# Kernel optimization log

Measured on AMD Instinct MI355X. Metric: run time of the kernel, lower is better.

The kernel has to match this reference:

```python
import jax, jax.numpy as jnp
import numpy as np

D_MODEL = 512
NHEAD = 8
HEAD_DIM = D_MODEL // NHEAD


def setup_inputs() -> dict:
    key = jax.random.key(0)
    k1, k2, k3, k4, k5 = jax.random.split(key, 5)
    x = jax.random.normal(k1, (4, 2048, D_MODEL), dtype=jnp.float32)
    s = 1.0 / np.sqrt(D_MODEL)
    W_qkv = jax.random.normal(k2, (D_MODEL, 3 * D_MODEL), dtype=jnp.float32) * s
    b_qkv = jax.random.normal(k3, (3 * D_MODEL,), dtype=jnp.float32) * 0.01
    W_fc = jax.random.normal(k4, (D_MODEL, D_MODEL), dtype=jnp.float32) * s
    b_fc = jax.random.normal(k5, (D_MODEL,), dtype=jnp.float32) * 0.01
    return {"x": x, "W_qkv": W_qkv, "b_qkv": b_qkv, "W_fc": W_fc, "b_fc": b_fc}


def reference(x, W_qkv, b_qkv, W_fc, b_fc):
    b, t, _ = x.shape
    qkv = x @ W_qkv + b_qkv                      # [b, t, 3*d]
    q, k, v = jnp.split(qkv, 3, axis=-1)
    def heads(a):
        return a.reshape(b, t, NHEAD, HEAD_DIM).transpose(0, 2, 1, 3)  # b h t d
    q, k, v = heads(q), heads(k), heads(v)
    scale = HEAD_DIM ** -0.5
    dots = jnp.einsum('bhid,bhjd->bhij', q, k) * scale
    attn = jax.nn.softmax(dots, axis=-1)         # dropout = identity (eval)
    out = jnp.einsum('bhij,bhjd->bhid', attn, v)
    out = out.transpose(0, 2, 1, 3).reshape(b, t, D_MODEL)
    return out @ W_fc + b_fc
```

## Files before the change

kernel.cpp:

```cpp
#include <hip/hip_runtime.h>
#include <hip/hip_bf16.h>
#include <cstddef>
#include <cstdint>

typedef __bf16 bf16_t;
typedef __attribute__((ext_vector_type(8))) __bf16 bf16x8;
typedef __attribute__((ext_vector_type(4))) float f32x4;
typedef __attribute__((ext_vector_type(16))) float f32x16;
typedef __attribute__((ext_vector_type(2))) unsigned uint2v;

#define B_   4
#define T_   2048
#define D_   512
#define H_   8
#define HD_  64
#define BT_  8192
#define N3_  1536

__device__ inline f32x4 mfma16(bf16x8 a, bf16x8 b, f32x4 c) {
  return __builtin_amdgcn_mfma_f32_16x16x32_bf16(a, b, c, 0, 0, 0);
}
__device__ inline f32x16 mfma32(bf16x8 a, bf16x8 b, f32x16 c) {
  return __builtin_amdgcn_mfma_f32_32x32x16_bf16(a, b, c, 0, 0, 0);
}

#define GLOADLDS(lds_base, gsrc)                                           \
  __builtin_amdgcn_global_load_lds(                                        \
      (const __attribute__((address_space(1))) unsigned int*)(gsrc),       \
      (__attribute__((address_space(3))) unsigned int*)(lds_base), 16, 0, 0)


__global__ __launch_bounds__(256) void k_castx(const float* __restrict__ in,
                                               bf16_t* __restrict__ out) {
  const size_t i = ((size_t)blockIdx.x * 256 + threadIdx.x) * 8;
  f32x4 v0 = *reinterpret_cast<const f32x4*>(&in[i]);
  f32x4 v1 = *reinterpret_cast<const f32x4*>(&in[i + 4]);
  bf16x8 o;
#pragma unroll
  for (int k = 0; k < 4; ++k) { o[k] = (bf16_t)v0[k]; o[4 + k] = (bf16_t)v1[k]; }
  *reinterpret_cast<bf16x8*>(&out[i]) = o;
}

__global__ __launch_bounds__(256) void k_tcast(const float* __restrict__ in,
                                               bf16_t* __restrict__ out,
                                               int R, int C) {
  __shared__ bf16_t tile[64][72];
  const int c0 = blockIdx.x * 64, r0 = blockIdx.y * 64;
  const int t = threadIdx.x;
  const int rr = t >> 4;
  const int cc = (t & 15) * 4;
#pragma unroll
  for (int p = 0; p < 4; ++p) {
    int r = p * 16 + rr;
    f32x4 v = *reinterpret_cast<const f32x4*>(&in[(size_t)(r0 + r) * C + c0 + cc]);
#pragma unroll
    for (int i = 0; i < 4; ++i) tile[cc + i][r] = (bf16_t)v[i];
  }
  __syncthreads();
#pragma unroll
  for (int p = 0; p < 4; ++p) {
    int c = p * 16 + rr;
    union { uint2 u; bf16_t e[4]; } pk;
#pragma unroll
    for (int i = 0; i < 4; ++i) pk.e[i] = tile[c][cc + i];
    *reinterpret_cast<uint2*>(&out[(size_t)(c0 + c) * R + r0 + cc]) = pk.u;
  }
}

__global__ __launch_bounds__(512) void k_gemm_qkv(
    const bf16_t* __restrict__ Xb, const bf16_t* __restrict__ Wt,
    const float* __restrict__ bias, bf16_t* __restrict__ Qp,
    bf16_t* __restrict__ Kp, bf16_t* __restrict__ Vp) {
  __shared__ __align__(16) char smem[34816];
  bf16_t* As = (bf16_t*)smem;
  bf16_t* Bs = (bf16_t*)(smem + 16384);
  const int bm0 = blockIdx.x * 128, bn0 = blockIdx.y * 128;
  const int tid = threadIdx.x, lane = tid & 63, wid = tid >> 6;
  const int wm = wid >> 1, wn = wid & 1;
  const int rl = lane >> 3;
  const int s8 = lane & 7;
  f32x4 acc[2][4] = {};
  for (int kt = 0; kt < D_; kt += 64) {
#pragma unroll
    for (int r = 0; r < 2; ++r) {
      const int row = 16 * wid + 8 * r + rl;
      const int sl = (s8 ^ (row & 7)) * 8;
      GLOADLDS(&As[(16 * wid + 8 * r) * 64],
               &Xb[(size_t)(bm0 + row) * D_ + kt + sl]);
      GLOADLDS(&Bs[(16 * wid + 8 * r) * 64],
               &Wt[(size_t)(bn0 + row) * D_ + kt + sl]);
    }
    __syncthreads();
    const int fr = lane & 15, kq8 = lane >> 4;
    bf16x8 af[2][2], bfr[4][2];
#pragma unroll
    for (int m = 0; m < 2; ++m) {
      const int row = wm * 32 + m * 16 + fr;
#pragma unroll
      for (int kh = 0; kh < 2; ++kh) {
        const int sL = kh * 4 + kq8;
        af[m][kh] = *reinterpret_cast<const bf16x8*>(
            &As[row * 64 + ((sL ^ (row & 7)) * 8)]);
      }
    }
#pragma unroll
    for (int n = 0; n < 4; ++n) {
      const int row = wn * 64 + n * 16 + fr;
#pragma unroll
      for (int kh = 0; kh < 2; ++kh) {
        const int sL = kh * 4 + kq8;
        bfr[n][kh] = *reinterpret_cast<const bf16x8*>(
            &Bs[row * 64 + ((sL ^ (row & 7)) * 8)]);
      }
    }
#pragma unroll
    for (int kh = 0; kh < 2; ++kh)
#pragma unroll
      for (int m = 0; m < 2; ++m)
#pragma unroll
        for (int n = 0; n < 4; ++n)
          acc[m][n] = mfma16(af[m][kh], bfr[n][kh], acc[m][n]);
    __syncthreads();
  }
  const float c1 = 0.18033688011112042f;
  const int fr = lane & 15, fq = lane >> 4;
  const int sec = bn0 >> 9;
  const int bb = bm0 >> 11, tt0 = bm0 & 2047;
  const int hb = (bn0 & 511) >> 6;
  bf16_t* Cs = (bf16_t*)smem;
  const int LDC = 136;
  if (sec < 2) {
#pragma unroll
    for (int n = 0; n < 4; ++n) {
      int col = wn * 64 + n * 16 + fr;
      float bv = bias[bn0 + col];
#pragma unroll
      for (int m = 0; m < 2; ++m) {
        int rbase = wm * 32 + m * 16 + fq * 4;
#pragma unroll
        for (int j = 0; j < 4; ++j) {
          float fv = acc[m][n][j] + bv;
          if (sec == 0) fv *= c1;
          Cs[(rbase + j) * LDC + col] = (bf16_t)fv;
        }
      }
    }
  } else {
#pragma unroll
    for (int n = 0; n < 4; ++n) {
      int col = wn * 64 + n * 16 + fr;
      float bv = bias[bn0 + col];
#pragma unroll
      for (int m = 0; m < 2; ++m) {
        int rbase = wm * 32 + m * 16 + fq * 4;
        union { uint2 u; bf16_t e[4]; } pk;
#pragma unroll
        for (int j = 0; j < 4; ++j) pk.e[j] = (bf16_t)(acc[m][n][j] + bv);
        *reinterpret_cast<uint2*>(&Cs[col * LDC + rbase]) = pk.u;
      }
    }
  }
  __syncthreads();
#pragma unroll
  for (int c = 0; c < 4; ++c) {
    const int chunk = wid * 4 + c;
    if (sec < 2) {
      const int h2 = chunk >> 4, rb = (chunk >> 2) & 3, dc = chunk & 3;
      bf16x8 v = *reinterpret_cast<const bf16x8*>(
          &Cs[(rb * 32 + (lane & 31)) * LDC + h2 * 64 + dc * 16 + (lane >> 5) * 8]);
      bf16_t* dst = sec == 0 ? Qp : Kp;
      size_t a = (((size_t)((bb * H_ + hb + h2) * 64 + (tt0 >> 5) + rb)) * 4 + dc) * 512 +
                 lane * 8;
      *reinterpret_cast<bf16x8*>(&dst[a]) = v;
    } else {
      const int h2 = chunk >> 4, tb = (chunk >> 1) & 7, dh = chunk & 1;
      bf16x8 v = *reinterpret_cast<const bf16x8*>(
          &Cs[(h2 * 64 + dh * 32 + (lane & 31)) * LDC + tb * 16 + (lane >> 5) * 8]);
      size_t a = (((size_t)((bb * H_ + hb + h2) * 128 + (tt0 >> 4) + tb)) * 2 + dh) * 512 +
                 lane * 8;
      *reinterpret_cast<bf16x8*>(&Vp[a]) = v;
    }
  }
}

__global__ __launch_bounds__(512) void k_gemm_fc(
    const bf16_t* __restrict__ A, const bf16_t* __restrict__ Wt,
    const float* __restrict__ bias, float* __restrict__ Out) {
  __shared__ __align__(16) bf16_t As[128 * 32];
  __shared__ __align__(16) bf16_t Bs[64 * 32];
  const int bm0 = blockIdx.x * 128, bn0 = blockIdx.y * 64;
  const int tid = threadIdx.x, lane = tid & 63, wid = tid >> 6;
  const int wm2 = wid >> 1, wn2 = wid & 1;
  const int srow = 16 * wid + (lane >> 2);
  const int scol = (lane & 3) * 8;
  f32x4 acc[2][2] = {};
  for (int kt = 0; kt < D_; kt += 32) {
    GLOADLDS(&As[(16 * wid) * 32], &A[(size_t)(bm0 + srow) * D_ + kt + scol]);
    if (wid < 4)
      GLOADLDS(&Bs[(16 * wid) * 32],
               &Wt[(size_t)(bn0 + 16 * wid + (lane >> 2)) * D_ + kt + scol]);
    __syncthreads();
    const int fr = lane & 15, kq = (lane >> 4) * 8;
    bf16x8 af[2], bfr[2];
#pragma unroll
    for (int m = 0; m < 2; ++m)
      af[m] = *reinterpret_cast<const bf16x8*>(&As[(wm2 * 32 + m * 16 + fr) * 32 + kq]);
#pragma unroll
    for (int n = 0; n < 2; ++n)
      bfr[n] = *reinterpret_cast<const bf16x8*>(&Bs[(wn2 * 32 + n * 16 + fr) * 32 + kq]);
#pragma unroll
    for (int m = 0; m < 2; ++m)
#pragma unroll
      for (int n = 0; n < 2; ++n)
        acc[m][n] = mfma16(af[m], bfr[n], acc[m][n]);
    __syncthreads();
  }
  const int fr = lane & 15, fq = lane >> 4;
#pragma unroll
  for (int n = 0; n < 2; ++n) {
    int ng = bn0 + wn2 * 32 + n * 16 + fr;
    float bv = bias[ng];
#pragma unroll
    for (int m = 0; m < 2; ++m) {
      int mg = bm0 + wm2 * 32 + m * 16 + fq * 4;
#pragma unroll
      for (int j = 0; j < 4; ++j)
        Out[(size_t)(mg + j) * D_ + ng] = acc[m][n][j] + bv;
    }
  }
}

__device__ __forceinline__ void loadKf(const bf16_t* __restrict__ b, int tile,
                                       bf16x8 (&kf)[4]) {
#pragma unroll
  for (int ds = 0; ds < 4; ++ds)
    kf[ds] = *reinterpret_cast<const bf16x8*>(b + ((size_t)(tile * 4 + ds) << 9));
}
__device__ __forceinline__ void loadVf(const bf16_t* __restrict__ b, int c0,
                                       bf16x8 (&v)[4]) {
  v[0] = *reinterpret_cast<const bf16x8*>(b + ((size_t)(c0 * 2 + 0) << 9));
  v[1] = *reinterpret_cast<const bf16x8*>(b + ((size_t)(c0 * 2 + 2) << 9));
  v[2] = *reinterpret_cast<const bf16x8*>(b + ((size_t)(c0 * 2 + 1) << 9));
  v[3] = *reinterpret_cast<const bf16x8*>(b + ((size_t)(c0 * 2 + 3) << 9));
}

__device__ __forceinline__ f32x16 qk32(const bf16x8 (&kf)[4],
                                       const bf16x8 (&qf)[4]) {
  f32x16 s;
#pragma unroll
  for (int i = 0; i < 16; ++i) s[i] = 0.f;
  s = mfma32(kf[0], qf[0], s);
  s = mfma32(kf[1], qf[1], s);
  s = mfma32(kf[2], qf[2], s);
  s = mfma32(kf[3], qf[3], s);
  return s;
}

__device__ __forceinline__ void pv_acc(f32x16& s, const bf16x8 (&v)[4],
                                       f32x16& o0, f32x16& o1, f32x16& lacc,
                                       bf16x8 ones) {
  float p[16];
#pragma unroll
  for (int r = 0; r < 16; ++r) p[r] = __builtin_exp2f(s[r]);
  union PW { __hip_bfloat162 h; unsigned u; };
#pragma unroll
  for (int ks = 0; ks < 2; ++ks) {
    const int rb = ks * 8;
    PW t0, t1, t2, t3;
    t0.h = __float22bfloat162_rn(make_float2(p[rb + 0], p[rb + 1]));
    t1.h = __float22bfloat162_rn(make_float2(p[rb + 2], p[rb + 3]));
    t2.h = __float22bfloat162_rn(make_float2(p[rb + 4], p[rb + 5]));
    t3.h = __float22bfloat162_rn(make_float2(p[rb + 6], p[rb + 7]));
    uint2v r02 = __builtin_amdgcn_permlane32_swap(t0.u, t2.u, false, false);
    uint2v r13 = __builtin_amdgcn_permlane32_swap(t1.u, t3.u, false, false);
    union { unsigned u[4]; bf16x8 vv; } af;
    af.u[0] = r02[0]; af.u[1] = r13[0]; af.u[2] = r02[1]; af.u[3] = r13[1];
    if (ks == 0) {
      o0 = mfma32(af.vv, v[0], o0);
      o1 = mfma32(af.vv, v[2], o1);
    } else {
      o0 = mfma32(af.vv, v[1], o0);
      o1 = mfma32(af.vv, v[3], o1);
    }
    lacc = mfma32(af.vv, ones, lacc);
  }
}

__global__ __launch_bounds__(512, 2) void k_attn(
    const bf16_t* __restrict__ Qp, const bf16_t* __restrict__ Kp,
    const bf16_t* __restrict__ Vp, bf16_t* __restrict__ Ctx) {
  __shared__ float Olds[4][32][64];
  __shared__ float Llds[4][16][64];
  const int lin = blockIdx.x;
  const int logical = (lin & 7) * 64 + (lin >> 3);
  const int bh = logical >> 4, qblk = logical & 15;
  const int tid = threadIdx.x, lane = tid & 63, wid = tid >> 6;
  const int qt = wid & 3, half = wid >> 2;
  const int q0 = qblk * 128 + qt * 32;
  const int tbase = half * 32;
  const bf16_t* Qb = Qp + ((size_t)(bh * 64 + (q0 >> 5)) << 11) + lane * 8;
  const bf16_t* Kb = Kp + ((size_t)bh << 17) + lane * 8;
  const bf16_t* Vb = Vp + ((size_t)bh << 17) + lane * 8;
  bf16x8 qf[4], ones;
#pragma unroll
  for (int ds = 0; ds < 4; ++ds)
    qf[ds] = *reinterpret_cast<const bf16x8*>(Qb + ((size_t)ds << 9));
#pragma unroll
  for (int i = 0; i < 8; ++i) ones[i] = (bf16_t)1.0f;
  f32x16 o0, o1, lacc;
#pragma unroll
  for (int i = 0; i < 16; ++i) { o0[i] = 0.f; o1[i] = 0.f; lacc[i] = 0.f; }
  bf16x8 kfA[4], kfB[4], vA[4], vB[4];
  loadKf(Kb, tbase + 0, kfA);
  loadKf(Kb, tbase + 1, kfB);
  loadVf(Vb, (tbase << 1) + 0, vA);
  loadVf(Vb, (tbase << 1) + 2, vB);
  f32x16 sA = qk32(kfA, qf);
  for (int st = 0; st < 32; st += 2) {
    const bool more = (st + 2 < 32);
    f32x16 sB = qk32(kfB, qf);
    if (more) loadKf(Kb, tbase + st + 2, kfA);
    pv_acc(sA, vA, o0, o1, lacc, ones);
    if (more) loadVf(Vb, ((tbase + st) << 1) + 4, vA);
    if (more) sA = qk32(kfA, qf);
    if (more) loadKf(Kb, tbase + st + 3, kfB);
    pv_acc(sB, vB, o0, o1, lacc, ones);
    if (more) loadVf(Vb, ((tbase + st) << 1) + 6, vB);
  }
  if (half == 1) {
#pragma unroll
    for (int r = 0; r < 16; ++r) {
      Olds[qt][r][lane] = o0[r];
      Olds[qt][16 + r][lane] = o1[r];
      Llds[qt][r][lane] = lacc[r];
    }
  }
  __syncthreads();
  if (half == 1) return;
  const int bb = bh >> 3, hh = bh & 7;
  const int ql = lane & 31;
#pragma unroll
  for (int r = 0; r < 16; ++r) {
    const int qr = (r & 3) + 8 * (r >> 2) + 4 * (lane >> 5);
    const float li =
        __builtin_amdgcn_rcpf(lacc[r] + Llds[qt][r][lane]);
    float v0 = (o0[r] + Olds[qt][r][lane]) * li;
    float v1 = (o1[r] + Olds[qt][16 + r][lane]) * li;
    size_t base = ((size_t)(bb * T_ + q0 + qr)) * D_ + hh * HD_ + ql;
    Ctx[base] = (bf16_t)v0;
    Ctx[base + 32] = (bf16_t)v1;
  }
}

extern "C" void kernel_launch(void* const* d_in, const int* in_sizes, int n_in,
                              void* d_out, int out_size, void* d_ws,
                              size_t ws_size, hipStream_t stream) {
  const float* x    = (const float*)d_in[0];
  const float* Wqkv = (const float*)d_in[1];
  const float* bqkv = (const float*)d_in[2];
  const float* Wfc  = (const float*)d_in[3];
  const float* bfc  = (const float*)d_in[4];
  float* out = (float*)d_out;

  char* ws = (char*)d_ws;
  size_t off = 0;
  bf16_t* Wqt = (bf16_t*)(ws + off); off += (size_t)N3_ * D_ * 2;
  bf16_t* Wft = (bf16_t*)(ws + off); off += (size_t)D_ * D_ * 2;
  bf16_t* Qb  = (bf16_t*)(ws + off); off += (size_t)BT_ * D_ * 2;
  bf16_t* Kb  = (bf16_t*)(ws + off); off += (size_t)BT_ * D_ * 2;
  bf16_t* Vb  = (bf16_t*)(ws + off); off += (size_t)BT_ * D_ * 2;
  bf16_t* Ctx = (bf16_t*)(ws + off); off += (size_t)BT_ * D_ * 2;
  bf16_t* Xb  = Ctx;

  k_castx<<<BT_ * D_ / (256 * 8), 256, 0, stream>>>(x, Xb);
  k_tcast<<<dim3(N3_ / 64, D_ / 64), 256, 0, stream>>>(Wqkv, Wqt, D_, N3_);
  k_tcast<<<dim3(D_ / 64, D_ / 64), 256, 0, stream>>>(Wfc, Wft, D_, D_);
  k_gemm_qkv<<<dim3(BT_ / 128, N3_ / 128), 512, 0, stream>>>(Xb, Wqt, bqkv, Qb,
                                                             Kb, Vb);
  k_attn<<<512, 512, 0, stream>>>(Qb, Kb, Vb, Ctx);
  k_gemm_fc<<<dim3(BT_ / 128, D_ / 64), 512, 0, stream>>>(Ctx, Wft, bfc, out);
}
```

Baseline: 99.35 us.

## Process two query tiles per wave and replace ones-MFMA row sum with VALU sum

New measurement: 115.0 us. +15.7%, slower.

```diff
diff --git a/kernel.cpp b/kernel.cpp
--- a/kernel.cpp
+++ b/kernel.cpp
@@ -257,11 +257,13 @@
 }
 
 __device__ __forceinline__ void pv_acc(f32x16& s, const bf16x8 (&v)[4],
-                                       f32x16& o0, f32x16& o1, f32x16& lacc,
-                                       bf16x8 ones) {
+                                       f32x16& o0, f32x16& o1, float& lsum) {
   float p[16];
 #pragma unroll
   for (int r = 0; r < 16; ++r) p[r] = __builtin_exp2f(s[r]);
+  lsum += (((p[0] + p[1]) + (p[2] + p[3])) + ((p[4] + p[5]) + (p[6] + p[7]))) +
+          (((p[8] + p[9]) + (p[10] + p[11])) +
+           ((p[12] + p[13]) + (p[14] + p[15])));
   union PW { __hip_bfloat162 h; unsigned u; };
 #pragma unroll
   for (int ks = 0; ks < 2; ++ks) {
@@ -282,73 +284,87 @@
       o0 = mfma32(af.vv, v[1], o0);
       o1 = mfma32(af.vv, v[3], o1);
     }
-    lacc = mfma32(af.vv, ones, lacc);
-  }
-}
-
-__global__ __launch_bounds__(512, 2) void k_attn(
+  }
+}
+
+__global__ __launch_bounds__(256, 1) void k_attn(
     const bf16_t* __restrict__ Qp, const bf16_t* __restrict__ Kp,
     const bf16_t* __restrict__ Vp, bf16_t* __restrict__ Ctx) {
-  __shared__ float Olds[4][32][64];
-  __shared__ float Llds[4][16][64];
+  __shared__ float Olds[2][64][64];
+  __shared__ float Llds[2][2][64];
   const int lin = blockIdx.x;
   const int logical = (lin & 7) * 64 + (lin >> 3);
   const int bh = logical >> 4, qblk = logical & 15;
   const int tid = threadIdx.x, lane = tid & 63, wid = tid >> 6;
-  const int qt = wid & 3, half = wid >> 2;
-  const int q0 = qblk * 128 + qt * 32;
+  const int qt = wid & 1, half = wid >> 1;
+  const int q0 = qblk * 128 + qt * 64;
   const int tbase = half * 32;
   const bf16_t* Qb = Qp + ((size_t)(bh * 64 + (q0 >> 5)) << 11) + lane * 8;
   const bf16_t* Kb = Kp + ((size_t)bh << 17) + lane * 8;
   const bf16_t* Vb = Vp + ((size_t)bh << 17) + lane * 8;
-  bf16x8 qf[4], ones;
-#pragma unroll
-  for (int ds = 0; ds < 4; ++ds)
-    qf[ds] = *reinterpret_cast<const bf16x8*>(Qb + ((size_t)ds << 9));
-#pragma unroll
-  for (int i = 0; i < 8; ++i) ones[i] = (bf16_t)1.0f;
-  f32x16 o0, o1, lacc;
-#pragma unroll
-  for (int i = 0; i < 16; ++i) { o0[i] = 0.f; o1[i] = 0.f; lacc[i] = 0.f; }
+  bf16x8 qf0[4], qf1[4];
+#pragma unroll
+  for (int ds = 0; ds < 4; ++ds) {
+    qf0[ds] = *reinterpret_cast<const bf16x8*>(Qb + ((size_t)ds << 9));
+    qf1[ds] = *reinterpret_cast<const bf16x8*>(Qb + ((size_t)(4 + ds) << 9));
+  }
+  f32x16 o00, o01, o10, o11;
+#pragma unroll
+  for (int i = 0; i < 16; ++i) {
+    o00[i] = 0.f; o01[i] = 0.f; o10[i] = 0.f; o11[i] = 0.f;
+  }
+  float lsum0 = 0.f, lsum1 = 0.f;
   bf16x8 kfA[4], kfB[4], vA[4], vB[4];
   loadKf(Kb, tbase + 0, kfA);
   loadKf(Kb, tbase + 1, kfB);
   loadVf(Vb, (tbase << 1) + 0, vA);
   loadVf(Vb, (tbase << 1) + 2, vB);
-  f32x16 sA = qk32(kfA, qf);
+  f32x16 sA0 = qk32(kfA, qf0);
+  f32x16 sA1 = qk32(kfA, qf1);
   for (int st = 0; st < 32; st += 2) {
     const bool more = (st + 2 < 32);
-    f32x16 sB = qk32(kfB, qf);
+    f32x16 sB0 = qk32(kfB, qf0);
     if (more) loadKf(Kb, tbase + st + 2, kfA);
-    pv_acc(sA, vA, o0, o1, lacc, ones);
+    pv_acc(sA0, vA, o00, o01, lsum0);
+    f32x16 sB1 = qk32(kfB, qf1);
+    pv_acc(sA1, vA, o10, o11, lsum1);
     if (more) loadVf(Vb, ((tbase + st) << 1) + 4, vA);
-    if (more) sA = qk32(kfA, qf);
-    if (more) loadKf(Kb, tbase + st + 3, kfB);
-    pv_acc(sB, vB, o0, o1, lacc, ones);
+    if (more) sA0 = qk32(kfA, qf0);
+    pv_acc(sB0, vB, o00, o01, lsum0);
+    if (more) { sA1 = qk32(kfA, qf1); loadKf(Kb, tbase + st + 3, kfB); }
+    pv_acc(sB1, vB, o10, o11, lsum1);
     if (more) loadVf(Vb, ((tbase + st) << 1) + 6, vB);
   }
+  lsum0 += __shfl_xor(lsum0, 32);
+  lsum1 += __shfl_xor(lsum1, 32);
   if (half == 1) {
 #pragma unroll
     for (int r = 0; r < 16; ++r) {
-      Olds[qt][r][lane] = o0[r];
-      Olds[qt][16 + r][lane] = o1[r];
-      Llds[qt][r][lane] = lacc[r];
-    }
+      Olds[qt][r][lane] = o00[r];
+      Olds[qt][16 + r][lane] = o01[r];
+      Olds[qt][32 + r][lane] = o10[r];
+      Olds[qt][48 + r][lane] = o11[r];
+    }
+    Llds[qt][0][lane] = lsum0;
+    Llds[qt][1][lane] = lsum1;
   }
   __syncthreads();
   if (half == 1) return;
+  const float linv0 = 1.f / (lsum0 + Llds[qt][0][lane]);
+  const float linv1 = 1.f / (lsum1 + Llds[qt][1][lane]);
   const int bb = bh >> 3, hh = bh & 7;
   const int ql = lane & 31;
 #pragma unroll
   for (int r = 0; r < 16; ++r) {
     const int qr = (r & 3) + 8 * (r >> 2) + 4 * (lane >> 5);
-    const float li =
-        __builtin_amdgcn_rcpf(lacc[r] + Llds[qt][r][lane]);
-    float v0 = (o0[r] + Olds[qt][r][lane]) * li;
-    float v1 = (o1[r] + Olds[qt][16 + r][lane]) * li;
-    size_t base = ((size_t)(bb * T_ + q0 + qr)) * D_ + hh * HD_ + ql;
-    Ctx[base] = (bf16_t)v0;
-    Ctx[base + 32] = (bf16_t)v1;
+    const float li0 = __shfl(linv0, qr);
+    const float li1 = __shfl(linv1, qr);
+    size_t base0 = ((size_t)(bb * T_ + q0 + qr)) * D_ + hh * HD_ + ql;
+    Ctx[base0] = (bf16_t)((o00[r] + Olds[qt][r][lane]) * li0);
+    Ctx[base0 + 32] = (bf16_t)((o01[r] + Olds[qt][16 + r][lane]) * li0);
+    size_t base1 = base0 + (size_t)32 * D_;
+    Ctx[base1] = (bf16_t)((o10[r] + Olds[qt][32 + r][lane]) * li1);
+    Ctx[base1 + 32] = (bf16_t)((o11[r] + Olds[qt][48 + r][lane]) * li1);
   }
 }
 
@@ -377,6 +393,6 @@
   k_tcast<<<dim3(D_ / 64, D_ / 64), 256, 0, stream>>>(Wfc, Wft, D_, D_);
   k_gemm_qkv<<<dim3(BT_ / 128, N3_ / 128), 512, 0, stream>>>(Xb, Wqt, bqkv, Qb,
                                                              Kb, Vb);
-  k_attn<<<512, 512, 0, stream>>>(Qb, Kb, Vb, Ctx);
+  k_attn<<<512, 256, 0, stream>>>(Qb, Kb, Vb, Ctx);
   k_gemm_fc<<<dim3(BT_ / 128, D_ / 64), 512, 0, stream>>>(Ctx, Wft, bfc, out);
 }
```
